# Kernel tuning notes

Measured on AMD Instinct MI355X. Metric: run time of the kernel, lower is better.

## Reference

```python
import jax, jax.numpy as jnp
import numpy as np

KD, KH, KW = 3, 3, 3
C = 64

def setup_inputs() -> dict:
    key = jax.random.key(0)
    kx, kw = jax.random.split(key)
    x = jax.random.normal(kx, (4, 16, 112, 112, C), dtype=jnp.float32)
    # One 3x3x3 filter per channel; DHWIO layout with I=in_per_group=1, O=C
    w = jax.random.normal(kw, (KD, KH, KW, 1, C), dtype=jnp.float32) * 0.1
    return {"x": x, "w": w}

def reference(x, w) -> jnp.ndarray:
    # Depthwise 3D conv: feature_group_count=C makes each output channel the
    # conv of the matching input channel with its own [3,3,3] kernel, which is
    # exactly the per-channel Conv3D(filters=1) loop + concat in the original.
    return jax.lax.conv_general_dilated(
        x, w,
        window_strides=(1, 1, 1),
        padding="SAME",
        dimension_numbers=("NDHWC", "DHWIO", "NDHWC"),
        feature_group_count=C,
    )
```

## Files before the change

### kernel.cpp

```cpp
#include <hip/hip_runtime.h>

#define N_ 4
#define D_ 16
#define H_ 112
#define W_ 112
#define C_ 64

#define DO_ 2
#define HO_ 2
#define DT_ (D_ / DO_)
#define HTILES (H_ / HO_)
#define WAVES_PER_BLOCK 4
#define HGROUPS (HTILES / WAVES_PER_BLOCK)
#define WSPLIT 4
#define WQ (W_ / WSPLIT)
#define NWG (N_ * DT_ * HGROUPS * WSPLIT)
#define CB (C_ * 4)

__device__ float zpage[W_ * C_];

__global__ __launch_bounds__(256, 4)
void dwconv3d_kernel(const float* __restrict__ x,
                     const float* __restrict__ wgt,
                     float* __restrict__ out) {
    int b = blockIdx.x;
    b = (b & 7) * (NWG / 8) + (b >> 3);
    const int wh = b % WSPLIT; b /= WSPLIT;
    const int hg = b % HGROUPS; b /= HGROUPS;
    const int dt = b % DT_;     b /= DT_;
    const int n  = b;

    const int c   = threadIdx.x & 63;
    const int wid = __builtin_amdgcn_readfirstlane(threadIdx.x >> 6);

    const int d0 = dt * DO_;
    const int h0 = (hg * WAVES_PER_BLOCK + wid) * HO_;
    const int w0 = wh * WQ;

    float wt[3][3][3];
#pragma unroll
    for (int kd = 0; kd < 3; ++kd)
#pragma unroll
      for (int kh = 0; kh < 3; ++kh)
#pragma unroll
        for (int kw = 0; kw < 3; ++kw)
          wt[kd][kh][kw] = wgt[((kd * 3 + kh) * 3 + kw) * C_ + c];

    const char* bx[4][4];
#pragma unroll
    for (int dr = 0; dr < 4; ++dr) {
      const int d = d0 - 1 + dr;
#pragma unroll
      for (int hr = 0; hr < 4; ++hr) {
        const int h = h0 - 1 + hr;
        if (d >= 0 && d < D_ && h >= 0 && h < H_)
          bx[dr][hr] = (const char*)(x + (size_t)((n * D_ + d) * H_ + h) * W_ * C_);
        else
          bx[dr][hr] = (const char*)zpage;
      }
    }

    char* ox[2][2];
#pragma unroll
    for (int od = 0; od < 2; ++od)
#pragma unroll
      for (int oh = 0; oh < 2; ++oh)
        ox[od][oh] = (char*)(out +
            (size_t)((n * D_ + d0 + od) * H_ + (h0 + oh)) * W_ * C_);

    unsigned vb = (unsigned)((w0 + 2) * CB) + (unsigned)(c * 4);

    float win[3][4][4];
#pragma unroll
    for (int dr = 0; dr < 4; ++dr)
#pragma unroll
      for (int hr = 0; hr < 4; ++hr) {
        win[1][dr][hr] = *(const float*)(bx[dr][hr] + (vb - 2 * CB));
        win[2][dr][hr] = *(const float*)(bx[dr][hr] + (vb - 1 * CB));
        win[0][dr][hr] = 0.0f;
      }
    if (w0 != 0) {
#pragma unroll
      for (int dr = 0; dr < 4; ++dr)
#pragma unroll
        for (int hr = 0; hr < 4; ++hr)
          win[0][dr][hr] = *(const float*)(bx[dr][hr] + (vb - 3 * CB));
    }

#pragma unroll 4
    for (int w = w0; w < w0 + WQ; ++w) {
      float nxt[4][4];
      if (w + 2 < W_) {
#pragma unroll
        for (int dr = 0; dr < 4; ++dr)
#pragma unroll
          for (int hr = 0; hr < 4; ++hr)
            nxt[dr][hr] = *(const float*)(bx[dr][hr] + vb);
      } else {
#pragma unroll
        for (int dr = 0; dr < 4; ++dr)
#pragma unroll
          for (int hr = 0; hr < 4; ++hr)
            nxt[dr][hr] = 0.0f;
      }

      float acc[2][2] = {{0.0f, 0.0f}, {0.0f, 0.0f}};
#pragma unroll
      for (int kw = 0; kw < 3; ++kw)
#pragma unroll
        for (int kd = 0; kd < 3; ++kd)
#pragma unroll
          for (int kh = 0; kh < 3; ++kh)
#pragma unroll
            for (int od = 0; od < 2; ++od)
#pragma unroll
              for (int oh = 0; oh < 2; ++oh)
                acc[od][oh] += win[kw][od + kd][oh + kh] * wt[kd][kh][kw];

#pragma unroll
      for (int od = 0; od < 2; ++od)
#pragma unroll
        for (int oh = 0; oh < 2; ++oh)
          *(float*)(ox[od][oh] + (vb - 2 * CB)) = acc[od][oh];

#pragma unroll
      for (int dr = 0; dr < 4; ++dr)
#pragma unroll
        for (int hr = 0; hr < 4; ++hr) {
          win[0][dr][hr] = win[1][dr][hr];
          win[1][dr][hr] = win[2][dr][hr];
          win[2][dr][hr] = nxt[dr][hr];
        }
      vb += CB;
    }
}

extern "C" void kernel_launch(void* const* d_in, const int* in_sizes, int n_in,
                              void* d_out, int out_size, void* d_ws, size_t ws_size,
                              hipStream_t stream) {
    const float* x   = (const float*)d_in[0];
    const float* wgt = (const float*)d_in[1];
    float* out = (float*)d_out;

    dim3 grid(NWG);
    dim3 block(256);
    dwconv3d_kernel<<<grid, block, 0, stream>>>(x, wgt, out);
}
```

Baseline: 372.9 us.

## Stream input columns into rotating accumulators instead of a sliding window

Replaces the 3-column register window, which held 48 floats and shifted every step, with a streaming scheme. Each newly loaded input column is immediately multiplied into three rotating sets of partial-sum accumulators, one per kw tap, and its register slot is refilled with the next load. This drops the window registers and the shift copies, so launch bounds are raised from 4 to 8 waves per SIMD to increase occupancy. In exchange the code is a fully unrolled, macro-heavy schedule with special prologue and epilogue handling at the W edges, which costs code size and is harder to verify.

```diff
diff --git a/kernel.cpp b/kernel.cpp
--- a/kernel.cpp
+++ b/kernel.cpp
@@ -19,7 +19,52 @@
 
 __device__ float zpage[W_ * C_];
 
-__global__ __launch_bounds__(256, 4)
+template <int U, int DR, int HR, int KWM>
+__device__ __forceinline__ void stream_fma(float (&acc)[3][2][2],
+                                           const float (&wt)[3][3][3],
+                                           float v) {
+  constexpr int iN = U % 3;
+  constexpr int iM = (U + 5) % 3;
+  constexpr int iO = (U + 4) % 3;
+#pragma unroll
+  for (int od = (DR >= 2 ? DR - 2 : 0); od <= (DR < 1 ? DR : 1); ++od)
+#pragma unroll
+    for (int oh = (HR >= 2 ? HR - 2 : 0); oh <= (HR < 1 ? HR : 1); ++oh) {
+      if (KWM & 1) acc[iN][od][oh] += v * wt[DR - od][HR - oh][0];
+      if (KWM & 2) acc[iM][od][oh] += v * wt[DR - od][HR - oh][1];
+      if (KWM & 4) acc[iO][od][oh] += v * wt[DR - od][HR - oh][2];
+    }
+}
+
+#define FL(U, M, DR, HR)                                        \
+  stream_fma<U, DR, HR, M>(acc, wt, pf[DR][HR]);                \
+  pf[DR][HR] = *(const float*)(bx[DR][HR] + vb);
+#define F_(U, M, DR, HR) stream_fma<U, DR, HR, M>(acc, wt, pf[DR][HR]);
+#define L_(DR, HR) pf[DR][HR] = *(const float*)(bx[DR][HR] + vb);
+
+#define FMA_LOAD_ALL(U, M)                                      \
+  FL(U,M,0,0) FL(U,M,0,1) FL(U,M,0,2) FL(U,M,0,3)               \
+  FL(U,M,1,0) FL(U,M,1,1) FL(U,M,1,2) FL(U,M,1,3)               \
+  FL(U,M,2,0) FL(U,M,2,1) FL(U,M,2,2) FL(U,M,2,3)               \
+  FL(U,M,3,0) FL(U,M,3,1) FL(U,M,3,2) FL(U,M,3,3)
+
+#define FMA_ALL(U, M)                                           \
+  F_(U,M,0,0) F_(U,M,0,1) F_(U,M,0,2) F_(U,M,0,3)               \
+  F_(U,M,1,0) F_(U,M,1,1) F_(U,M,1,2) F_(U,M,1,3)               \
+  F_(U,M,2,0) F_(U,M,2,1) F_(U,M,2,2) F_(U,M,2,3)               \
+  F_(U,M,3,0) F_(U,M,3,1) F_(U,M,3,2) F_(U,M,3,3)
+
+#define LOAD_ALL()                                              \
+  L_(0,0) L_(0,1) L_(0,2) L_(0,3) L_(1,0) L_(1,1) L_(1,2) L_(1,3) \
+  L_(2,0) L_(2,1) L_(2,2) L_(2,3) L_(3,0) L_(3,1) L_(3,2) L_(3,3)
+
+#define STORE4(U)                                                             \
+  *(float*)(ox[0][0] + (vb - 2*CB)) = acc[(U+4)%3][0][0]; acc[(U+4)%3][0][0] = 0.f; \
+  *(float*)(ox[0][1] + (vb - 2*CB)) = acc[(U+4)%3][0][1]; acc[(U+4)%3][0][1] = 0.f; \
+  *(float*)(ox[1][0] + (vb - 2*CB)) = acc[(U+4)%3][1][0]; acc[(U+4)%3][1][0] = 0.f; \
+  *(float*)(ox[1][1] + (vb - 2*CB)) = acc[(U+4)%3][1][1]; acc[(U+4)%3][1][1] = 0.f;
+
+__global__ __launch_bounds__(256, 8)
 void dwconv3d_kernel(const float* __restrict__ x,
                      const float* __restrict__ wgt,
                      float* __restrict__ out) {
@@ -68,71 +113,55 @@
         ox[od][oh] = (char*)(out +
             (size_t)((n * D_ + d0 + od) * H_ + (h0 + oh)) * W_ * C_);
 
-    unsigned vb = (unsigned)((w0 + 2) * CB) + (unsigned)(c * 4);
+    float pf[4][4];
+    float acc[3][2][2];
+#pragma unroll
+    for (int i = 0; i < 3; ++i)
+#pragma unroll
+      for (int od = 0; od < 2; ++od)
+#pragma unroll
+        for (int oh = 0; oh < 2; ++oh) acc[i][od][oh] = 0.f;
 
-    float win[3][4][4];
-#pragma unroll
-    for (int dr = 0; dr < 4; ++dr)
-#pragma unroll
-      for (int hr = 0; hr < 4; ++hr) {
-        win[1][dr][hr] = *(const float*)(bx[dr][hr] + (vb - 2 * CB));
-        win[2][dr][hr] = *(const float*)(bx[dr][hr] + (vb - 1 * CB));
-        win[0][dr][hr] = 0.0f;
-      }
-    if (w0 != 0) {
+    unsigned vb = (unsigned)(w0 * CB) + (unsigned)(c * 4);
+    const bool wend = (w0 + WQ < W_);
+
+    if (w0) {
 #pragma unroll
       for (int dr = 0; dr < 4; ++dr)
 #pragma unroll
         for (int hr = 0; hr < 4; ++hr)
-          win[0][dr][hr] = *(const float*)(bx[dr][hr] + (vb - 3 * CB));
+          pf[dr][hr] = *(const float*)(bx[dr][hr] + (vb - CB));
+      FMA_LOAD_ALL(0, 1)
+    } else {
+      LOAD_ALL()
     }
-
-#pragma unroll 4
-    for (int w = w0; w < w0 + WQ; ++w) {
-      float nxt[4][4];
-      if (w + 2 < W_) {
-#pragma unroll
-        for (int dr = 0; dr < 4; ++dr)
-#pragma unroll
-          for (int hr = 0; hr < 4; ++hr)
-            nxt[dr][hr] = *(const float*)(bx[dr][hr] + vb);
-      } else {
-#pragma unroll
-        for (int dr = 0; dr < 4; ++dr)
-#pragma unroll
-          for (int hr = 0; hr < 4; ++hr)
-            nxt[dr][hr] = 0.0f;
-      }
-
-      float acc[2][2] = {{0.0f, 0.0f}, {0.0f, 0.0f}};
-#pragma unroll
-      for (int kw = 0; kw < 3; ++kw)
-#pragma unroll
-        for (int kd = 0; kd < 3; ++kd)
-#pragma unroll
-          for (int kh = 0; kh < 3; ++kh)
-#pragma unroll
-            for (int od = 0; od < 2; ++od)
-#pragma unroll
-              for (int oh = 0; oh < 2; ++oh)
-                acc[od][oh] += win[kw][od + kd][oh + kh] * wt[kd][kh][kw];
-
-#pragma unroll
-      for (int od = 0; od < 2; ++od)
-#pragma unroll
-        for (int oh = 0; oh < 2; ++oh)
-          *(float*)(ox[od][oh] + (vb - 2 * CB)) = acc[od][oh];
-
-#pragma unroll
-      for (int dr = 0; dr < 4; ++dr)
-#pragma unroll
-        for (int hr = 0; hr < 4; ++hr) {
-          win[0][dr][hr] = win[1][dr][hr];
-          win[1][dr][hr] = win[2][dr][hr];
-          win[2][dr][hr] = nxt[dr][hr];
-        }
-      vb += CB;
+    vb += CB;
+    FMA_LOAD_ALL(1, 3) vb += CB;
+    FMA_LOAD_ALL(2, 7) STORE4(2) vb += CB;
+    FMA_LOAD_ALL(3, 7) STORE4(3) vb += CB;
+    FMA_LOAD_ALL(4, 7) STORE4(4) vb += CB;
+    FMA_LOAD_ALL(5, 7) STORE4(5) vb += CB;
+#pragma unroll 1
+    for (int it = 0; it < 3; ++it) {
+      FMA_LOAD_ALL(0, 7) STORE4(0) vb += CB;
+      FMA_LOAD_ALL(1, 7) STORE4(1) vb += CB;
+      FMA_LOAD_ALL(2, 7) STORE4(2) vb += CB;
+      FMA_LOAD_ALL(3, 7) STORE4(3) vb += CB;
+      FMA_LOAD_ALL(4, 7) STORE4(4) vb += CB;
+      FMA_LOAD_ALL(5, 7) STORE4(5) vb += CB;
     }
+    FMA_LOAD_ALL(0, 7) STORE4(0) vb += CB;
+    FMA_LOAD_ALL(1, 7) STORE4(1) vb += CB;
+    FMA_LOAD_ALL(2, 7) STORE4(2) vb += CB;
+    FMA_LOAD_ALL(3, 7) STORE4(3) vb += CB;
+    if (wend) {
+      FMA_LOAD_ALL(4, 6)
+    } else {
+      FMA_ALL(4, 6)
+    }
+    STORE4(4) vb += CB;
+    if (wend) { FMA_ALL(5, 4) }
+    STORE4(5)
 }
 
 extern "C" void kernel_launch(void* const* d_in, const int* in_sizes, int n_in,
```

Result: slower. 866.7 us (+132.4%).
